# Kernel tuning notes

Measured on AMD Instinct MI355X. Metric: run time of the kernel, lower is better.

The kernel has to match this reference:

```python
import jax, jax.numpy as jnp
import numpy as np

B, S, D, H = 1, 2048, 1024, 16
HD = D // H
S_SLOPE = 10.0      # soft_thres_layer s
C_MASK = -10000.0   # soft_thres_layer c == masked_bias
ALPHA = 0.0         # config.threshold
W_STD = 0.02        # GPT2 init std for weights


def setup_inputs() -> dict:
    key = jax.random.key(0)
    k1, k2, k3 = jax.random.split(key, 3)
    return {
        "hidden_states": jax.random.normal(k1, (B, S, D), dtype=jnp.float32),
        "c_attn_w": jax.random.normal(k2, (D, 3 * D), dtype=jnp.float32) * W_STD,
        "c_attn_b": jnp.zeros((3 * D,), dtype=jnp.float32),
        "c_proj_w": jax.random.normal(k3, (D, D), dtype=jnp.float32) * W_STD,
        "c_proj_b": jnp.zeros((D,), dtype=jnp.float32),
    }


def reference(hidden_states, c_attn_w, c_attn_b, c_proj_w, c_proj_b):
    # Conv1D: x @ w + b (GPT2 convention: weight is [in, out])
    qkv = hidden_states @ c_attn_w + c_attn_b            # [B,S,3D]
    q, k, v = jnp.split(qkv, 3, axis=-1)

    def split_heads(x):
        return x.reshape(B, S, H, HD).transpose(0, 2, 1, 3)  # [B,H,S,hd]

    q, k, v = split_heads(q), split_heads(k), split_heads(v)

    # prun path: NO 1/sqrt(d) scaling (skipped when self.prun is True)
    w = jnp.einsum("bhqd,bhkd->bhqk", q, k)              # [B,H,S,S]

    causal = jnp.tril(jnp.ones((S, S), dtype=bool))[None, None]
    w = jnp.where(causal, w, C_MASK)

    # soft-threshold pruning: smoothly pushes scores below alpha toward c=-10000
    w = C_MASK + (w - C_MASK) * jax.nn.sigmoid(S_SLOPE * (w - ALPHA))

    a = jax.nn.softmax(w, axis=-1)                        # attn_dropout = identity (eval)
    out = jnp.einsum("bhqk,bhkd->bhqd", a, v)             # [B,H,S,hd]
    out = out.transpose(0, 2, 1, 3).reshape(B, S, D)      # merge heads
    return out @ c_proj_w + c_proj_b                      # resid_dropout = identity
```

## Files before the change

kernel.cpp:

```cpp
#include <hip/hip_runtime.h>


#define S_LEN 2048
#define DM    1024
#define NH    16
#define HD    64
#define SLOPE 10.0f
#define CMASK -10000.0f
#define SP    2080

typedef short s16x4 __attribute__((ext_vector_type(4)));
typedef short s16x8 __attribute__((ext_vector_type(8)));
typedef float f32x4 __attribute__((ext_vector_type(4)));

#define MFMA16(a,b,c) __builtin_amdgcn_mfma_f32_16x16x32_bf16(a,b,c,0,0,0)
#define GLDS16(g,l) __builtin_amdgcn_global_load_lds( \
    (const __attribute__((address_space(1))) void*)(g), \
    (__attribute__((address_space(3))) void*)(l), 16, 0, 0)

__device__ __forceinline__ short f2bf(float f){
    unsigned u = __float_as_uint(f);
    u += 0x7fffu + ((u >> 16) & 1u);
    return (short)(u >> 16);
}
__device__ __forceinline__ float bf2f(short x){
    return __uint_as_float(((unsigned)(unsigned short)x) << 16);
}
struct bfpair { short hi, lo; };
__device__ __forceinline__ bfpair split_bf(float x){
    bfpair r; r.hi = f2bf(x);
    r.lo = f2bf(x - bf2f(r.hi));
    return r;
}

template<int ROWS, int THREADS>
__device__ __forceinline__ void stage_tile(const short* gbase, int rstride,
                                           short* lds, int tid){
#pragma unroll
    for (int it = 0; it < ROWS*8/THREADS; ++it){
        int s = it*THREADS + tid;
        int row = s >> 3, grp = s & 7;
        const short* src = gbase + (size_t)row*rstride + ((grp ^ (row & 7)) << 3);
        GLDS16(src, lds + (size_t)s*8);
    }
}
__device__ __forceinline__ s16x8 frag(const short* lds, int row, int kg){
    return *(const s16x8*)&lds[row*64 + ((kg ^ (row & 7)) << 3)];
}

template<bool SPLIT, int OUT>
__global__ __launch_bounds__(256)
void gemm_s(const short* __restrict__ Ahg, const short* __restrict__ Alg,
            const short* __restrict__ Bhg, const short* __restrict__ Blg,
            const float* __restrict__ bias,
            short* __restrict__ o0, short* __restrict__ o1,
            float* __restrict__ of)
{
    __shared__ __align__(16) short Ah_s[128*64];
    __shared__ __align__(16) short Bh_s[128*64];
    __shared__ __align__(16) short Al_s[SPLIT ? 128*64 : 8];
    __shared__ __align__(16) short Bl_s[SPLIT ? 128*64 : 8];

    const int tid = threadIdx.x, lane = tid & 63, wid = tid >> 6;
    const int lr = lane & 15, lg = lane >> 4;
    const int brow = blockIdx.y*128, bcol = blockIdx.x*128;
    const int wm = (wid >> 1)*64, wn = (wid & 1)*64;

    f32x4 acc[4][4];
#pragma unroll
    for (int m = 0; m < 4; ++m)
#pragma unroll
        for (int n = 0; n < 4; ++n) acc[m][n] = (f32x4){0.f,0.f,0.f,0.f};

    for (int k0 = 0; k0 < DM; k0 += 64){
        stage_tile<128,256>(Ahg + (size_t)brow*DM + k0, DM, Ah_s, tid);
        stage_tile<128,256>(Bhg + (size_t)bcol*DM + k0, DM, Bh_s, tid);
        if constexpr (SPLIT){
            stage_tile<128,256>(Alg + (size_t)brow*DM + k0, DM, Al_s, tid);
            stage_tile<128,256>(Blg + (size_t)bcol*DM + k0, DM, Bl_s, tid);
        }
        __syncthreads();
#pragma unroll
        for (int kc = 0; kc < 2; ++kc){
            s16x8 ah[4], al[4], bh[4], bl[4];
#pragma unroll
            for (int m = 0; m < 4; ++m){
                ah[m] = frag(Ah_s, wm + m*16 + lr, kc*4 + lg);
                if constexpr (SPLIT) al[m] = frag(Al_s, wm + m*16 + lr, kc*4 + lg);
            }
#pragma unroll
            for (int n = 0; n < 4; ++n){
                bh[n] = frag(Bh_s, wn + n*16 + lr, kc*4 + lg);
                if constexpr (SPLIT) bl[n] = frag(Bl_s, wn + n*16 + lr, kc*4 + lg);
            }
#pragma unroll
            for (int m = 0; m < 4; ++m)
#pragma unroll
                for (int n = 0; n < 4; ++n){
                    acc[m][n] = MFMA16(ah[m], bh[n], acc[m][n]);
                    if constexpr (SPLIT){
                        acc[m][n] = MFMA16(ah[m], bl[n], acc[m][n]);
                        acc[m][n] = MFMA16(al[m], bh[n], acc[m][n]);
                    }
                }
        }
        __syncthreads();
    }

#pragma unroll
    for (int m = 0; m < 4; ++m)
#pragma unroll
        for (int n = 0; n < 4; ++n){
            int row  = brow + wm + m*16 + lg*4;
            int gcol = bcol + wn + n*16 + lr;
            float bv = bias[gcol];
            int h0 = gcol >> 6, d = gcol & 63;
#pragma unroll
            for (int v = 0; v < 4; ++v){
                float val = acc[m][n][v] + bv;
                if constexpr (OUT == 0){
                    bfpair p = split_bf(val);
                    size_t o = ((size_t)h0*S_LEN + row + v)*HD + d;
                    o0[o] = p.hi; o1[o] = p.lo;
                } else if constexpr (OUT == 1){
                    o0[((size_t)h0*S_LEN + row + v)*HD + d] = f2bf(val);
                } else if constexpr (OUT == 2){
                    o0[(size_t)(row + v)*DM + gcol] = f2bf(val);
                } else {
                    of[(size_t)(row + v)*DM + gcol] = val;
                }
            }
        }
}

__global__ __launch_bounds__(256)
void split_f32(const float* __restrict__ x, short* __restrict__ h,
               short* __restrict__ l, int n4)
{
    int i = blockIdx.x*256 + threadIdx.x;
    if (i >= n4) return;
    float4 v = *(const float4*)&x[(size_t)i*4];
    bfpair a = split_bf(v.x), b = split_bf(v.y), c = split_bf(v.z), d = split_bf(v.w);
    s16x4 hv, lv;
    hv.x = a.hi; hv.y = b.hi; hv.z = c.hi; hv.w = d.hi;
    lv.x = a.lo; lv.y = b.lo; lv.z = c.lo; lv.w = d.lo;
    *(s16x4*)&h[(size_t)i*4] = hv;
    *(s16x4*)&l[(size_t)i*4] = lv;
}

template<bool SPL>
__global__ __launch_bounds__(256)
void wtrans(const float* __restrict__ W, int N, short* __restrict__ Th,
            short* __restrict__ Tl)
{
    __shared__ float t[64][65];
    const int tid = threadIdx.x;
    const int tn = blockIdx.x*64, tk = blockIdx.y*64;
#pragma unroll
    for (int it = 0; it < 4; ++it){
        int idx = tid + it*256;
        int r = idx >> 4, c4 = (idx & 15)*4;
        float4 v = *(const float4*)&W[(size_t)(tk + r)*N + tn + c4];
        t[r][c4] = v.x; t[r][c4+1] = v.y; t[r][c4+2] = v.z; t[r][c4+3] = v.w;
    }
    __syncthreads();
#pragma unroll
    for (int it = 0; it < 4; ++it){
        int idx = tid + it*256;
        int n = idx >> 4, c4 = (idx & 15)*4;
        s16x4 hv, lv;
#pragma unroll
        for (int j = 0; j < 4; ++j){
            bfpair p = split_bf(t[c4+j][n]);
            hv[j] = p.hi; lv[j] = p.lo;
        }
        *(s16x4*)&Th[(size_t)(tn + n)*DM + tk + c4] = hv;
        if constexpr (SPL) *(s16x4*)&Tl[(size_t)(tn + n)*DM + tk + c4] = lv;
    }
}

__global__ __launch_bounds__(256)
void vtrans(const short* __restrict__ Vb, short* __restrict__ Vt)
{
    __shared__ short t[64][66];
    const int tid = threadIdx.x;
    const int td = blockIdx.x*64, ts = blockIdx.y*64;
#pragma unroll
    for (int it = 0; it < 4; ++it){
        int idx = tid + it*256;
        int r = idx >> 4, c4 = (idx & 15)*4;
        s16x4 v = *(const s16x4*)&Vb[(size_t)(ts + r)*DM + td + c4];
        t[r][c4] = v.x; t[r][c4+1] = v.y; t[r][c4+2] = v.z; t[r][c4+3] = v.w;
    }
    __syncthreads();
#pragma unroll
    for (int it = 0; it < 4; ++it){
        int idx = tid + it*256;
        int n = idx >> 4, c4 = (idx & 15)*4;
        s16x4 o;
#pragma unroll
        for (int j = 0; j < 4; ++j) o[j] = t[c4+j][n];
        *(s16x4*)&Vt[(size_t)(td + n)*SP + ts + c4] = o;
    }
}

__global__ __launch_bounds__(64)
void sv_partial(const short* __restrict__ Vb, float* __restrict__ PB)
{
    int b = blockIdx.x, h = blockIdx.y, d = threadIdx.x;
    float s = 0.f;
#pragma unroll 8
    for (int k = 0; k < 64; ++k)
        s += bf2f(Vb[(size_t)(b*64 + k)*DM + h*HD + d]);
    PB[((size_t)h*32 + b)*64 + d] = s;
}
__global__ __launch_bounds__(64)
void sv_suffix(const float* __restrict__ PB, float* __restrict__ SSV)
{
    int h = blockIdx.x, d = threadIdx.x;
    float s = 0.f;
    SSV[((size_t)h*33 + 32)*64 + d] = 0.f;
    for (int b = 31; b >= 0; --b){
        s += PB[((size_t)h*32 + b)*64 + d];
        SSV[((size_t)h*33 + b)*64 + d] = s;
    }
}

__global__ __launch_bounds__(128)
void attn_fwd(const short* __restrict__ QHh, const short* __restrict__ QHl,
              const short* __restrict__ KH, const short* __restrict__ Vt,
              const float* __restrict__ SSV, short* __restrict__ O)
{
    __shared__ __align__(16) short Ps[2][16*72];
    __shared__ float mrg[64][24];

    const int id = blockIdx.x;
    const int h  = (id & 7) + 8*((id >> 3) & 1);
    const int qt = 127 - (id >> 4);
    const int diag = qt >> 2;

    const int tid = threadIdx.x, lane = tid & 63, wid = tid >> 6;
    const int lr = lane & 15, lg = lane >> 4;
    const int qrow = qt*16 + lg*4;

    const short* qbh = QHh + ((size_t)h*S_LEN + qt*16)*HD;
    const short* qbl = QHl + ((size_t)h*S_LEN + qt*16)*HD;
    s16x8 aqh[2], aql[2];
#pragma unroll
    for (int kc = 0; kc < 2; ++kc){
        aqh[kc] = *(const s16x8*)&qbh[lr*HD + kc*32 + lg*8];
        aql[kc] = *(const s16x8*)&qbl[lr*HD + kc*32 + lg*8];
    }

    float m_run[4], l_run[4];
    f32x4 acc_o[4];
#pragma unroll
    for (int v = 0; v < 4; ++v){ m_run[v] = -1e30f; l_run[v] = 0.f; }
#pragma unroll
    for (int n = 0; n < 4; ++n) acc_o[n] = (f32x4){0.f,0.f,0.f,0.f};

    const short* kb0 = KH + (size_t)h*S_LEN*HD;
    const short* vb0 = Vt + (size_t)(h*HD)*SP;

    s16x8 bkc[2][4];
    if (wid <= diag){
        const short* kb = kb0 + (size_t)(wid*64)*HD;
#pragma unroll
        for (int kc = 0; kc < 2; ++kc)
#pragma unroll
            for (int n = 0; n < 4; ++n)
                bkc[kc][n] = *(const s16x8*)&kb[(n*16 + lr)*HD + kc*32 + lg*8];
    }

    for (int kvb = wid; kvb <= diag; kvb += 2){
        s16x8 bkn[2][4];
        if (kvb + 2 <= diag){
            const short* kb = kb0 + (size_t)((kvb+2)*64)*HD;
#pragma unroll
            for (int kc = 0; kc < 2; ++kc)
#pragma unroll
                for (int n = 0; n < 4; ++n)
                    bkn[kc][n] = *(const s16x8*)&kb[(n*16 + lr)*HD + kc*32 + lg*8];
        }

        f32x4 sc[4];
#pragma unroll
        for (int n = 0; n < 4; ++n) sc[n] = (f32x4){0.f,0.f,0.f,0.f};
#pragma unroll
        for (int kc = 0; kc < 2; ++kc)
#pragma unroll
            for (int n = 0; n < 4; ++n){
                sc[n] = MFMA16(aqh[kc], bkc[kc][n], sc[n]);
                sc[n] = MFMA16(aql[kc], bkc[kc][n], sc[n]);
            }

        const short* vb = vb0 + kvb*64;
        s16x8 bv0[4], bv1[4];
#pragma unroll
        for (int n = 0; n < 4; ++n){
            bv0[n] = *(const s16x8*)&vb[(size_t)(16*n + lr)*SP + lg*8];
            bv1[n] = *(const s16x8*)&vb[(size_t)(16*n + lr)*SP + 32 + lg*8];
        }

        float p[4][4], tmax[4];
#pragma unroll
        for (int v = 0; v < 4; ++v) tmax[v] = -1e30f;
        if (kvb == diag){
#pragma unroll
            for (int n = 0; n < 4; ++n){
                int key = kvb*64 + n*16 + lr;
#pragma unroll
                for (int v = 0; v < 4; ++v){
                    float w;
                    if (key > qrow + v) w = CMASK;
                    else {
                        float sv = sc[n][v];
                        float sig = 1.f / (1.f + __expf(-SLOPE*sv));
                        w = CMASK + (sv - CMASK)*sig;
                    }
                    p[n][v] = w;
                    tmax[v] = fmaxf(tmax[v], w);
                }
            }
        } else {
#pragma unroll
            for (int n = 0; n < 4; ++n)
#pragma unroll
                for (int v = 0; v < 4; ++v){
                    float sv = sc[n][v];
                    float sig = 1.f / (1.f + __expf(-SLOPE*sv));
                    float w = CMASK + (sv - CMASK)*sig;
                    p[n][v] = w;
                    tmax[v] = fmaxf(tmax[v], w);
                }
        }
#pragma unroll
        for (int v = 0; v < 4; ++v)
#pragma unroll
            for (int msk = 1; msk < 16; msk <<= 1)
                tmax[v] = fmaxf(tmax[v], __shfl_xor(tmax[v], msk, 64));

        float scale[4], rsum[4];
#pragma unroll
        for (int v = 0; v < 4; ++v){
            float mn = fmaxf(m_run[v], tmax[v]);
            scale[v] = __expf(m_run[v] - mn);
            m_run[v] = mn;
            rsum[v] = 0.f;
        }
#pragma unroll
        for (int n = 0; n < 4; ++n)
#pragma unroll
            for (int v = 0; v < 4; ++v){
                float e = __expf(p[n][v] - m_run[v]);
                p[n][v] = e;
                rsum[v] += e;
            }
#pragma unroll
        for (int v = 0; v < 4; ++v){
#pragma unroll
            for (int msk = 1; msk < 16; msk <<= 1)
                rsum[v] += __shfl_xor(rsum[v], msk, 64);
            l_run[v] = l_run[v]*scale[v] + rsum[v];
        }
#pragma unroll
        for (int n = 0; n < 4; ++n)
#pragma unroll
            for (int v = 0; v < 4; ++v) acc_o[n][v] *= scale[v];

#pragma unroll
        for (int n = 0; n < 4; ++n)
#pragma unroll
            for (int v = 0; v < 4; ++v)
                Ps[wid][(lg*4 + v)*72 + 16*n + lr] = f2bf(p[n][v]);
        asm volatile("s_waitcnt lgkmcnt(0)" ::: "memory");

        s16x8 pa0 = *(const s16x8*)&Ps[wid][lr*72 + lg*8];
        s16x8 pa1 = *(const s16x8*)&Ps[wid][lr*72 + 32 + lg*8];
#pragma unroll
        for (int n = 0; n < 4; ++n){
            acc_o[n] = MFMA16(pa0, bv0[n], acc_o[n]);
            acc_o[n] = MFMA16(pa1, bv1[n], acc_o[n]);
        }

#pragma unroll
        for (int kc = 0; kc < 2; ++kc)
#pragma unroll
            for (int n = 0; n < 4; ++n) bkc[kc][n] = bkn[kc][n];
    }

    if (wid == 1){
#pragma unroll
        for (int v = 0; v < 4; ++v){
            mrg[lane][v] = m_run[v];
            mrg[lane][4 + v] = l_run[v];
        }
#pragma unroll
        for (int n = 0; n < 4; ++n)
#pragma unroll
            for (int v = 0; v < 4; ++v) mrg[lane][8 + n*4 + v] = acc_o[n][v];
    }
    __syncthreads();
    if (wid != 0) return;

    {
        float e0[4], e1[4];
#pragma unroll
        for (int v = 0; v < 4; ++v){
            float m1 = mrg[lane][v], l1 = mrg[lane][4 + v];
            float mn = fmaxf(m_run[v], m1);
            e0[v] = __expf(m_run[v] - mn);
            e1[v] = __expf(m1 - mn);
            l_run[v] = l_run[v]*e0[v] + l1*e1[v];
            m_run[v] = mn;
        }
#pragma unroll
        for (int n = 0; n < 4; ++n)
#pragma unroll
            for (int v = 0; v < 4; ++v)
                acc_o[n][v] = acc_o[n][v]*e0[v] + mrg[lane][8 + n*4 + v]*e1[v];
    }

    {
        const float* sv = SSV + ((size_t)h*33 + (diag + 1))*64;
        float F = (float)(S_LEN - 64*(diag + 1));
        float e[4];
#pragma unroll
        for (int v = 0; v < 4; ++v){
            e[v] = __expf(CMASK - m_run[v]);
            l_run[v] += e[v]*F;
        }
#pragma unroll
        for (int n = 0; n < 4; ++n){
            float svv = sv[16*n + lr];
#pragma unroll
            for (int v = 0; v < 4; ++v) acc_o[n][v] += e[v]*svv;
        }
    }

#pragma unroll
    for (int n = 0; n < 4; ++n)
#pragma unroll
        for (int v = 0; v < 4; ++v){
            int row = qt*16 + lg*4 + v;
            int col = h*HD + 16*n + lr;
            O[(size_t)row*DM + col] = f2bf(acc_o[n][v] / l_run[v]);
        }
}

extern "C" void kernel_launch(void* const* d_in, const int* in_sizes, int n_in,
                              void* d_out, int out_size, void* d_ws, size_t ws_size,
                              hipStream_t stream)
{
    (void)in_sizes; (void)n_in; (void)out_size; (void)ws_size;
    const float* hs   = (const float*)d_in[0];
    const float* wqkv = (const float*)d_in[1];
    const float* bqkv = (const float*)d_in[2];
    const float* wprj = (const float*)d_in[3];
    const float* bprj = (const float*)d_in[4];

    char* p = (char*)d_ws;
    short* Ahg  = (short*)(p + (0ull  << 20));
    short* Alg  = (short*)(p + (4ull  << 20));
    short* WqTh = (short*)(p + (8ull  << 20));
    short* WqTl = (short*)(p + (14ull << 20));
    short* QHh  = (short*)(p + (20ull << 20));
    short* QHl  = (short*)(p + (24ull << 20));
    short* KH   = (short*)(p + (28ull << 20));
    short* Vbg  = (short*)(p + (32ull << 20));
    short* VT   = (short*)(p + (36ull << 20));
    float* PB   = (float*)(p + (41ull << 20));
    float* SSV  = (float*)(p + (42ull << 20));
    short* O    = Ahg;
    short* WpT  = WqTh;

    split_f32<<<S_LEN*DM/4/256, 256, 0, stream>>>(hs, Ahg, Alg, S_LEN*DM/4);
    wtrans<true><<<dim3(3*DM/64, DM/64), 256, 0, stream>>>(wqkv, 3*DM, WqTh, WqTl);

    gemm_s<true, 0><<<dim3(8, 16), 256, 0, stream>>>(
        Ahg, Alg, WqTh, WqTl, bqkv, QHh, QHl, nullptr);
    gemm_s<false, 1><<<dim3(8, 16), 256, 0, stream>>>(
        Ahg, nullptr, WqTh + (size_t)DM*DM, nullptr, bqkv + DM, KH, nullptr, nullptr);
    gemm_s<false, 2><<<dim3(8, 16), 256, 0, stream>>>(
        Ahg, nullptr, WqTh + (size_t)2*DM*DM, nullptr, bqkv + 2*DM, Vbg, nullptr, nullptr);

    wtrans<false><<<dim3(DM/64, DM/64), 256, 0, stream>>>(wprj, DM, WpT, nullptr);
    vtrans<<<dim3(DM/64, S_LEN/64), 256, 0, stream>>>(Vbg, VT);
    sv_partial<<<dim3(32, NH), 64, 0, stream>>>(Vbg, PB);
    sv_suffix<<<NH, 64, 0, stream>>>(PB, SSV);

    attn_fwd<<<2048, 128, 0, stream>>>(QHh, QHl, KH, VT, SSV, O);

    gemm_s<false, 3><<<dim3(8, 16), 256, 0, stream>>>(
        O, nullptr, WpT, nullptr, bprj, nullptr, nullptr, (float*)d_out);
}
```

Measured before the change: 185.6 us.

## Split causal attention into KV chunks with separate merge kernel; fuse QKV GEMMs

Replaces the two-wave-per-query-tile attention kernel with a split-KV scheme. Single-wave jobs each process up to 8 KV blocks, and a separate merge kernel combines the partial results using the stored max and sum values plus the masked-tail suffix term. This is meant to balance the triangular causal workload across many more blocks. The three QKV GEMM launches are also fused into one launch whose grid covers all three sections and branches on which section it is in. The cost is extra global traffic for the bf16 partial accumulators, which reuse dead workspace buffers, an extra launch, and some added precision loss from rounding partials to bf16.

```diff
diff --git a/kernel.cpp b/kernel.cpp
--- a/kernel.cpp
+++ b/kernel.cpp
@@ -48,18 +48,99 @@
     return *(const s16x8*)&lds[row*64 + ((kg ^ (row & 7)) << 3)];
 }
 
-template<bool SPLIT, int OUT>
 __global__ __launch_bounds__(256)
-void gemm_s(const short* __restrict__ Ahg, const short* __restrict__ Alg,
-            const short* __restrict__ Bhg, const short* __restrict__ Blg,
-            const float* __restrict__ bias,
-            short* __restrict__ o0, short* __restrict__ o1,
-            float* __restrict__ of)
+void gemm_qkv(const short* __restrict__ Ahg, const short* __restrict__ Alg,
+              const short* __restrict__ Bhg, const short* __restrict__ Blg,
+              const float* __restrict__ bias,
+              short* __restrict__ QHh, short* __restrict__ QHl,
+              short* __restrict__ KH,  short* __restrict__ Vb)
 {
     __shared__ __align__(16) short Ah_s[128*64];
     __shared__ __align__(16) short Bh_s[128*64];
-    __shared__ __align__(16) short Al_s[SPLIT ? 128*64 : 8];
-    __shared__ __align__(16) short Bl_s[SPLIT ? 128*64 : 8];
+    __shared__ __align__(16) short Al_s[128*64];
+    __shared__ __align__(16) short Bl_s[128*64];
+
+    const int tid = threadIdx.x, lane = tid & 63, wid = tid >> 6;
+    const int lr = lane & 15, lg = lane >> 4;
+    const int brow = blockIdx.y*128, bcol = blockIdx.x*128;
+    const int sec = bcol >> 10;
+    const int wm = (wid >> 1)*64, wn = (wid & 1)*64;
+
+    f32x4 acc[4][4];
+#pragma unroll
+    for (int m = 0; m < 4; ++m)
+#pragma unroll
+        for (int n = 0; n < 4; ++n) acc[m][n] = (f32x4){0.f,0.f,0.f,0.f};
+
+    for (int k0 = 0; k0 < DM; k0 += 64){
+        stage_tile<128,256>(Ahg + (size_t)brow*DM + k0, DM, Ah_s, tid);
+        stage_tile<128,256>(Bhg + (size_t)bcol*DM + k0, DM, Bh_s, tid);
+        if (sec == 0){
+            stage_tile<128,256>(Alg + (size_t)brow*DM + k0, DM, Al_s, tid);
+            stage_tile<128,256>(Blg + (size_t)bcol*DM + k0, DM, Bl_s, tid);
+        }
+        __syncthreads();
+#pragma unroll
+        for (int kc = 0; kc < 2; ++kc){
+            s16x8 ah[4], al[4], bh[4], bl[4];
+#pragma unroll
+            for (int m = 0; m < 4; ++m)
+                ah[m] = frag(Ah_s, wm + m*16 + lr, kc*4 + lg);
+#pragma unroll
+            for (int n = 0; n < 4; ++n)
+                bh[n] = frag(Bh_s, wn + n*16 + lr, kc*4 + lg);
+            if (sec == 0){
+#pragma unroll
+                for (int m = 0; m < 4; ++m)
+                    al[m] = frag(Al_s, wm + m*16 + lr, kc*4 + lg);
+#pragma unroll
+                for (int n = 0; n < 4; ++n)
+                    bl[n] = frag(Bl_s, wn + n*16 + lr, kc*4 + lg);
+            }
+#pragma unroll
+            for (int m = 0; m < 4; ++m)
+#pragma unroll
+                for (int n = 0; n < 4; ++n){
+                    acc[m][n] = MFMA16(ah[m], bh[n], acc[m][n]);
+                    if (sec == 0){
+                        acc[m][n] = MFMA16(ah[m], bl[n], acc[m][n]);
+                        acc[m][n] = MFMA16(al[m], bh[n], acc[m][n]);
+                    }
+                }
+        }
+        __syncthreads();
+    }
+
+#pragma unroll
+    for (int m = 0; m < 4; ++m)
+#pragma unroll
+        for (int n = 0; n < 4; ++n){
+            int row  = brow + wm + m*16 + lg*4;
+            int gcol = bcol + wn + n*16 + lr;
+            float bv = bias[gcol];
+            int h0 = (gcol & 1023) >> 6, d = gcol & 63;
+#pragma unroll
+            for (int v = 0; v < 4; ++v){
+                float val = acc[m][n][v] + bv;
+                if (sec == 0){
+                    bfpair p = split_bf(val);
+                    size_t o = ((size_t)h0*S_LEN + row + v)*HD + d;
+                    QHh[o] = p.hi; QHl[o] = p.lo;
+                } else if (sec == 1){
+                    KH[((size_t)h0*S_LEN + row + v)*HD + d] = f2bf(val);
+                } else {
+                    Vb[(size_t)(row + v)*DM + (gcol & 1023)] = f2bf(val);
+                }
+            }
+        }
+}
+
+__global__ __launch_bounds__(256)
+void gemm_proj(const short* __restrict__ Ahg, const short* __restrict__ Bhg,
+               const float* __restrict__ bias, float* __restrict__ C)
+{
+    __shared__ __align__(16) short Ah_s[128*64];
+    __shared__ __align__(16) short Bh_s[128*64];
 
     const int tid = threadIdx.x, lane = tid & 63, wid = tid >> 6;
     const int lr = lane & 15, lg = lane >> 4;
@@ -75,34 +156,21 @@
     for (int k0 = 0; k0 < DM; k0 += 64){
         stage_tile<128,256>(Ahg + (size_t)brow*DM + k0, DM, Ah_s, tid);
         stage_tile<128,256>(Bhg + (size_t)bcol*DM + k0, DM, Bh_s, tid);
-        if constexpr (SPLIT){
-            stage_tile<128,256>(Alg + (size_t)brow*DM + k0, DM, Al_s, tid);
-            stage_tile<128,256>(Blg + (size_t)bcol*DM + k0, DM, Bl_s, tid);
-        }
         __syncthreads();
 #pragma unroll
         for (int kc = 0; kc < 2; ++kc){
-            s16x8 ah[4], al[4], bh[4], bl[4];
-#pragma unroll
-            for (int m = 0; m < 4; ++m){
+            s16x8 ah[4], bh[4];
+#pragma unroll
+            for (int m = 0; m < 4; ++m)
                 ah[m] = frag(Ah_s, wm + m*16 + lr, kc*4 + lg);
-                if constexpr (SPLIT) al[m] = frag(Al_s, wm + m*16 + lr, kc*4 + lg);
-            }
-#pragma unroll
-            for (int n = 0; n < 4; ++n){
+#pragma unroll
+            for (int n = 0; n < 4; ++n)
                 bh[n] = frag(Bh_s, wn + n*16 + lr, kc*4 + lg);
-                if constexpr (SPLIT) bl[n] = frag(Bl_s, wn + n*16 + lr, kc*4 + lg);
-            }
 #pragma unroll
             for (int m = 0; m < 4; ++m)
 #pragma unroll
-                for (int n = 0; n < 4; ++n){
+                for (int n = 0; n < 4; ++n)
                     acc[m][n] = MFMA16(ah[m], bh[n], acc[m][n]);
-                    if constexpr (SPLIT){
-                        acc[m][n] = MFMA16(ah[m], bl[n], acc[m][n]);
-                        acc[m][n] = MFMA16(al[m], bh[n], acc[m][n]);
-                    }
-                }
         }
         __syncthreads();
     }
@@ -114,22 +182,9 @@
             int row  = brow + wm + m*16 + lg*4;
             int gcol = bcol + wn + n*16 + lr;
             float bv = bias[gcol];
-            int h0 = gcol >> 6, d = gcol & 63;
-#pragma unroll
-            for (int v = 0; v < 4; ++v){
-                float val = acc[m][n][v] + bv;
-                if constexpr (OUT == 0){
-                    bfpair p = split_bf(val);
-                    size_t o = ((size_t)h0*S_LEN + row + v)*HD + d;
-                    o0[o] = p.hi; o1[o] = p.lo;
-                } else if constexpr (OUT == 1){
-                    o0[((size_t)h0*S_LEN + row + v)*HD + d] = f2bf(val);
-                } else if constexpr (OUT == 2){
-                    o0[(size_t)(row + v)*DM + gcol] = f2bf(val);
-                } else {
-                    of[(size_t)(row + v)*DM + gcol] = val;
-                }
-            }
+#pragma unroll
+            for (int v = 0; v < 4; ++v)
+                C[(size_t)(row + v)*DM + gcol] = acc[m][n][v] + bv;
         }
 }
 
@@ -175,7 +230,8 @@
             hv[j] = p.hi; lv[j] = p.lo;
         }
         *(s16x4*)&Th[(size_t)(tn + n)*DM + tk + c4] = hv;
-        if constexpr (SPL) *(s16x4*)&Tl[(size_t)(tn + n)*DM + tk + c4] = lv;
+        if (SPL && tn < DM)
+            *(s16x4*)&Tl[(size_t)(tn + n)*DM + tk + c4] = lv;
     }
 }
 
@@ -226,21 +282,27 @@
     }
 }
 
-__global__ __launch_bounds__(128)
-void attn_fwd(const short* __restrict__ QHh, const short* __restrict__ QHl,
-              const short* __restrict__ KH, const short* __restrict__ Vt,
-              const float* __restrict__ SSV, short* __restrict__ O)
-{
-    __shared__ __align__(16) short Ps[2][16*72];
-    __shared__ float mrg[64][24];
-
-    const int id = blockIdx.x;
-    const int h  = (id & 7) + 8*((id >> 3) & 1);
-    const int qt = 127 - (id >> 4);
+__global__ __launch_bounds__(64)
+void attn_chunk(const short* __restrict__ QHh, const short* __restrict__ QHl,
+                const short* __restrict__ KH, const short* __restrict__ Vt,
+                short* __restrict__ acc0, short* __restrict__ acc1,
+                short* __restrict__ acc2, float* __restrict__ ML)
+{
+    __shared__ __align__(16) short Ps[16*72];
+
+    const int j = blockIdx.x;
+    const int h = (j & 7) + 8*((j >> 3) & 1);
+    const int t = j >> 4;
+    const int g = (t < 32) ? 0 : (t < 96) ? 1 : (t < 192) ? 2 : 3;
+    const int u = t - 16*g*(g+1);
+    const int qd = u / (g+1);
+    const int qt = 32*g + qd;
+    const int chunk = u - qd*(g+1);
     const int diag = qt >> 2;
-
-    const int tid = threadIdx.x, lane = tid & 63, wid = tid >> 6;
-    const int lr = lane & 15, lg = lane >> 4;
+    const int kv0 = chunk*8;
+    const int kv1 = min(kv0 + 8, diag + 1);
+
+    const int lane = threadIdx.x, lr = lane & 15, lg = lane >> 4;
     const int qrow = qt*16 + lg*4;
 
     const short* qbh = QHh + ((size_t)h*S_LEN + qt*16)*HD;
@@ -262,26 +324,14 @@
     const short* kb0 = KH + (size_t)h*S_LEN*HD;
     const short* vb0 = Vt + (size_t)(h*HD)*SP;
 
-    s16x8 bkc[2][4];
-    if (wid <= diag){
-        const short* kb = kb0 + (size_t)(wid*64)*HD;
+    for (int kvb = kv0; kvb < kv1; ++kvb){
+        const short* kb = kb0 + (size_t)(kvb*64)*HD;
+        s16x8 bk[2][4];
 #pragma unroll
         for (int kc = 0; kc < 2; ++kc)
 #pragma unroll
             for (int n = 0; n < 4; ++n)
-                bkc[kc][n] = *(const s16x8*)&kb[(n*16 + lr)*HD + kc*32 + lg*8];
-    }
-
-    for (int kvb = wid; kvb <= diag; kvb += 2){
-        s16x8 bkn[2][4];
-        if (kvb + 2 <= diag){
-            const short* kb = kb0 + (size_t)((kvb+2)*64)*HD;
-#pragma unroll
-            for (int kc = 0; kc < 2; ++kc)
-#pragma unroll
-                for (int n = 0; n < 4; ++n)
-                    bkn[kc][n] = *(const s16x8*)&kb[(n*16 + lr)*HD + kc*32 + lg*8];
-        }
+                bk[kc][n] = *(const s16x8*)&kb[(n*16 + lr)*HD + kc*32 + lg*8];
 
         f32x4 sc[4];
 #pragma unroll
@@ -290,8 +340,8 @@
         for (int kc = 0; kc < 2; ++kc)
 #pragma unroll
             for (int n = 0; n < 4; ++n){
-                sc[n] = MFMA16(aqh[kc], bkc[kc][n], sc[n]);
-                sc[n] = MFMA16(aql[kc], bkc[kc][n], sc[n]);
+                sc[n] = MFMA16(aqh[kc], bk[kc][n], sc[n]);
+                sc[n] = MFMA16(aql[kc], bk[kc][n], sc[n]);
             }
 
         const short* vb = vb0 + kvb*64;
@@ -372,80 +422,72 @@
         for (int n = 0; n < 4; ++n)
 #pragma unroll
             for (int v = 0; v < 4; ++v)
-                Ps[wid][(lg*4 + v)*72 + 16*n + lr] = f2bf(p[n][v]);
+                Ps[(lg*4 + v)*72 + 16*n + lr] = f2bf(p[n][v]);
         asm volatile("s_waitcnt lgkmcnt(0)" ::: "memory");
 
-        s16x8 pa0 = *(const s16x8*)&Ps[wid][lr*72 + lg*8];
-        s16x8 pa1 = *(const s16x8*)&Ps[wid][lr*72 + 32 + lg*8];
+        s16x8 pa0 = *(const s16x8*)&Ps[lr*72 + lg*8];
+        s16x8 pa1 = *(const s16x8*)&Ps[lr*72 + 32 + lg*8];
 #pragma unroll
         for (int n = 0; n < 4; ++n){
             acc_o[n] = MFMA16(pa0, bv0[n], acc_o[n]);
             acc_o[n] = MFMA16(pa1, bv1[n], acc_o[n]);
         }
-
-#pragma unroll
-        for (int kc = 0; kc < 2; ++kc)
-#pragma unroll
-            for (int n = 0; n < 4; ++n) bkc[kc][n] = bkn[kc][n];
-    }
-
-    if (wid == 1){
+    }
+
+    short* ab = (j < 2048) ? acc0 + (size_t)j*1024
+              : (j < 3072) ? acc1 + (size_t)(j-2048)*1024
+                           : acc2 + (size_t)(j-3072)*1024;
+#pragma unroll
+    for (int n = 0; n < 4; ++n)
+#pragma unroll
+        for (int v = 0; v < 4; ++v)
+            ab[(lg*4 + v)*64 + 16*n + lr] = f2bf(acc_o[n][v]);
+    if (lr == 0){
 #pragma unroll
         for (int v = 0; v < 4; ++v){
-            mrg[lane][v] = m_run[v];
-            mrg[lane][4 + v] = l_run[v];
-        }
-#pragma unroll
-        for (int n = 0; n < 4; ++n)
-#pragma unroll
-            for (int v = 0; v < 4; ++v) mrg[lane][8 + n*4 + v] = acc_o[n][v];
-    }
-    __syncthreads();
-    if (wid != 0) return;
-
-    {
-        float e0[4], e1[4];
-#pragma unroll
-        for (int v = 0; v < 4; ++v){
-            float m1 = mrg[lane][v], l1 = mrg[lane][4 + v];
-            float mn = fmaxf(m_run[v], m1);
-            e0[v] = __expf(m_run[v] - mn);
-            e1[v] = __expf(m1 - mn);
-            l_run[v] = l_run[v]*e0[v] + l1*e1[v];
-            m_run[v] = mn;
-        }
-#pragma unroll
-        for (int n = 0; n < 4; ++n)
-#pragma unroll
-            for (int v = 0; v < 4; ++v)
-                acc_o[n][v] = acc_o[n][v]*e0[v] + mrg[lane][8 + n*4 + v]*e1[v];
-    }
-
-    {
-        const float* sv = SSV + ((size_t)h*33 + (diag + 1))*64;
-        float F = (float)(S_LEN - 64*(diag + 1));
-        float e[4];
-#pragma unroll
-        for (int v = 0; v < 4; ++v){
-            e[v] = __expf(CMASK - m_run[v]);
-            l_run[v] += e[v]*F;
-        }
-#pragma unroll
-        for (int n = 0; n < 4; ++n){
-            float svv = sv[16*n + lr];
-#pragma unroll
-            for (int v = 0; v < 4; ++v) acc_o[n][v] += e[v]*svv;
-        }
-    }
-
-#pragma unroll
-    for (int n = 0; n < 4; ++n)
-#pragma unroll
-        for (int v = 0; v < 4; ++v){
-            int row = qt*16 + lg*4 + v;
-            int col = h*HD + 16*n + lr;
-            O[(size_t)row*DM + col] = f2bf(acc_o[n][v] / l_run[v]);
-        }
+            ML[((size_t)j*16 + lg*4 + v)*2 + 0] = m_run[v];
+            ML[((size_t)j*16 + lg*4 + v)*2 + 1] = l_run[v];
+        }
+    }
+}
+
+__global__ __launch_bounds__(64)
+void attn_merge(const short* __restrict__ acc0, const short* __restrict__ acc1,
+                const short* __restrict__ acc2, const float* __restrict__ ML,
+                const float* __restrict__ SSV, short* __restrict__ O)
+{
+    const int b = blockIdx.x;
+    const int h = b & 15, qt = b >> 4;
+    const int d = threadIdx.x;
+    const int g = qt >> 5, C = g + 1;
+    const int tbase = (g + 1)*(qt - 16*g);
+    const int diag = qt >> 2;
+    const float F = (float)(S_LEN - 64*(diag + 1));
+    const float svd = SSV[((size_t)h*33 + (diag + 1))*64 + d];
+
+    for (int r = 0; r < 16; ++r){
+        float M = -1e30f;
+        for (int c = 0; c < C; ++c){
+            int job = (tbase + c)*16 + h;
+            M = fmaxf(M, ML[((size_t)job*16 + r)*2]);
+        }
+        float num = 0.f, den = 0.f;
+        for (int c = 0; c < C; ++c){
+            int job = (tbase + c)*16 + h;
+            float m = ML[((size_t)job*16 + r)*2];
+            float l = ML[((size_t)job*16 + r)*2 + 1];
+            const short* ab = (job < 2048) ? acc0 + (size_t)job*1024
+                            : (job < 3072) ? acc1 + (size_t)(job-2048)*1024
+                                           : acc2 + (size_t)(job-3072)*1024;
+            float e = __expf(m - M);
+            num += e * bf2f(ab[r*64 + d]);
+            den += e * l;
+        }
+        float et = __expf(CMASK - M);
+        num += et * svd;
+        den += et * F;
+        O[(size_t)(qt*16 + r)*DM + h*64 + d] = f2bf(num/den);
+    }
 }
 
 extern "C" void kernel_launch(void* const* d_in, const int* in_sizes, int n_in,
@@ -464,33 +506,30 @@
     short* Alg  = (short*)(p + (4ull  << 20));
     short* WqTh = (short*)(p + (8ull  << 20));
     short* WqTl = (short*)(p + (14ull << 20));
-    short* QHh  = (short*)(p + (20ull << 20));
-    short* QHl  = (short*)(p + (24ull << 20));
-    short* KH   = (short*)(p + (28ull << 20));
-    short* Vbg  = (short*)(p + (32ull << 20));
-    short* VT   = (short*)(p + (36ull << 20));
-    float* PB   = (float*)(p + (41ull << 20));
-    float* SSV  = (float*)(p + (42ull << 20));
+    short* QHh  = (short*)(p + (16ull << 20));
+    short* QHl  = (short*)(p + (20ull << 20));
+    short* KH   = (short*)(p + (24ull << 20));
+    short* Vbg  = (short*)(p + (28ull << 20));
+    short* VT   = (short*)(p + (32ull << 20));
+    float* PB   = (float*)(p + (38ull << 20));
+    float* SSV  = (float*)(p + (38ull << 20) + (256ull << 10));
+    float* ML   = (float*)(p + (39ull << 20));
     short* O    = Ahg;
     short* WpT  = WqTh;
 
     split_f32<<<S_LEN*DM/4/256, 256, 0, stream>>>(hs, Ahg, Alg, S_LEN*DM/4);
     wtrans<true><<<dim3(3*DM/64, DM/64), 256, 0, stream>>>(wqkv, 3*DM, WqTh, WqTl);
 
-    gemm_s<true, 0><<<dim3(8, 16), 256, 0, stream>>>(
-        Ahg, Alg, WqTh, WqTl, bqkv, QHh, QHl, nullptr);
-    gemm_s<false, 1><<<dim3(8, 16), 256, 0, stream>>>(
-        Ahg, nullptr, WqTh + (size_t)DM*DM, nullptr, bqkv + DM, KH, nullptr, nullptr);
-    gemm_s<false, 2><<<dim3(8, 16), 256, 0, stream>>>(
-        Ahg, nullptr, WqTh + (size_t)2*DM*DM, nullptr, bqkv + 2*DM, Vbg, nullptr, nullptr);
+    gemm_qkv<<<dim3(24, 16), 256, 0, stream>>>(
+        Ahg, Alg, WqTh, WqTl, bqkv, QHh, QHl, KH, Vbg);
 
     wtrans<false><<<dim3(DM/64, DM/64), 256, 0, stream>>>(wprj, DM, WpT, nullptr);
     vtrans<<<dim3(DM/64, S_LEN/64), 256, 0, stream>>>(Vbg, VT);
     sv_partial<<<dim3(32, NH), 64, 0, stream>>>(Vbg, PB);
     sv_suffix<<<NH, 64, 0, stream>>>(PB, SSV);
 
-    attn_fwd<<<2048, 128, 0, stream>>>(QHh, QHl, KH, VT, SSV, O);
-
-    gemm_s<false, 3><<<dim3(8, 16), 256, 0, stream>>>(
-        O, nullptr, WpT, nullptr, bprj, nullptr, nullptr, (float*)d_out);
-}
+    attn_chunk<<<5120, 64, 0, stream>>>(QHh, QHl, KH, VT, Alg, WqTl, Vbg, ML);
+    attn_merge<<<2048, 64, 0, stream>>>(Alg, WqTl, Vbg, ML, SSV, O);
+
+    gemm_proj<<<dim3(8, 16), 256, 0, stream>>>(O, WpT, bprj, (float*)d_out);
+}
```

Result: no change. 182.1 us (-1.9%).
